# Optimization experiments

Measured on AMD Instinct MI355X. Metric: run time of the kernel, lower is better.

Reference implementation:

```python
import jax, jax.numpy as jnp
import numpy as np

B, N, DIN = 1, 1024, 512
NF, DCOND, H = 4, 128, 8
HD = DIN // H


def layernorm(x, g, b, eps=1e-5):
    mu = jnp.mean(x, axis=-1, keepdims=True)
    var = jnp.var(x, axis=-1, keepdims=True)
    return (x - mu) * jax.lax.rsqrt(var + eps) * g + b


def modlin2d(x, code, w_c, ln_g, ln_b, W, b):
    # code: [dcond, nf]; w_c: [din, dcond] -> code_mod: [nf, 1, din]
    code_mod = layernorm((w_c @ code).T, ln_g, ln_b)[:, None, :]
    return jnp.matmul(x * code_mod, W.T) + b


def setup_inputs() -> dict:
    key = jax.random.key(0)
    ks = jax.random.split(key, 8)
    s = lambda d: 1.0 / np.sqrt(d)
    return {
        "x": jax.random.normal(ks[0], (B, N, DIN), jnp.float32),
        "compatibility": jax.random.uniform(ks[1], (B, NF, N), jnp.float32),
        "code": jax.random.normal(ks[2], (DCOND, NF), jnp.float32),
        "w_c": jax.random.normal(ks[3], (DIN, DCOND), jnp.float32) * s(DCOND),
        "W_qkv": jax.random.normal(ks[4], (3 * DIN, DIN), jnp.float32) * s(DIN),
        "b_qkv": jnp.zeros((3 * DIN,), jnp.float32),
        "W_proj": jax.random.normal(ks[5], (DIN, DIN), jnp.float32) * s(DIN),
        "b_proj": jnp.zeros((DIN,), jnp.float32),
        "ln_qkv_g": jnp.ones((DIN,), jnp.float32),
        "ln_qkv_b": jnp.zeros((DIN,), jnp.float32),
        "ln_proj_g": jnp.ones((DIN,), jnp.float32),
        "ln_proj_b": jnp.zeros((DIN,), jnp.float32),
    }


def reference(x, compatibility, code, w_c, W_qkv, b_qkv, W_proj, b_proj,
              ln_qkv_g, ln_qkv_b, ln_proj_g, ln_proj_b):
    b, n, e = x.shape
    hd = e // H
    scale = hd ** -0.5
    # QKV: [B, nf, N, 3*din] -> split into [3, B, H, nf, N, hd]
    qkv = modlin2d(x[:, None, :, :], code, w_c, ln_qkv_g, ln_qkv_b, W_qkv, b_qkv)
    qkv = qkv.reshape(b, NF, n, 3, H, hd).transpose(3, 0, 4, 1, 2, 5)
    q, k, v = qkv[0], qkv[1], qkv[2]
    # first softmax over scaled scores
    attn = jax.nn.softmax(jnp.einsum('bhfnd,bhfmd->bhfnm', q, k) * scale, axis=-1)
    # compatibility outer product: [B, N, N] (sums over function axis)
    compat = jnp.einsum('bfn,bfm->bnm', compatibility, compatibility)
    W_hat = attn * compat[:, None, None, :, :]
    # second softmax
    Wm = jax.nn.softmax(W_hat, axis=-1)
    y_hat = jnp.einsum('bhfnm,bhfmd->bhfnd', Wm, v)
    y_hat = y_hat.transpose(0, 2, 3, 1, 4).reshape(b, NF, n, e)
    y = modlin2d(y_hat, code, w_c, ln_proj_g, ln_proj_b, W_proj, b_proj)
    return y
```

## Files before the change

kernel.cpp:

```cpp
#include <hip/hip_runtime.h>
#include <hip/hip_bf16.h>
#include <math.h>

#define NTOK 1024
#define DIN  512
#define NF   4
#define DCOND 128
#define H    8
#define HD   64
#define NQKV 1536

typedef __attribute__((ext_vector_type(8))) short bf16x8;
typedef __attribute__((ext_vector_type(4))) float f32x4;
typedef __attribute__((ext_vector_type(4))) unsigned short us4;

__device__ __forceinline__ unsigned short f2b(float f) {
  union { float f; unsigned int u; } v; v.f = f;
  unsigned int r = v.u + 0x7fffu + ((v.u >> 16) & 1u);
  return (unsigned short)(r >> 16);
}

__device__ __forceinline__ float b2f(unsigned short h) {
  union { unsigned int u; float f; } v; v.u = ((unsigned int)h) << 16;
  return v.f;
}

__device__ __forceinline__ void gl_lds16(const void* g, void* l) {
  __builtin_amdgcn_global_load_lds(
      (const __attribute__((address_space(1))) unsigned int*)g,
      (__attribute__((address_space(3))) unsigned int*)l, 16, 0, 0);
}

__global__ void ln_kernel(const float* __restrict__ code, const float* __restrict__ w_c,
                          const float* __restrict__ lnqg, const float* __restrict__ lnqb,
                          const float* __restrict__ lnpg, const float* __restrict__ lnpb,
                          float* __restrict__ cmq, float* __restrict__ cmp_) {
  const int i = threadIdx.x;
  const int w = i >> 6, lane = i & 63;
  float t[NF] = {0.f, 0.f, 0.f, 0.f};
  const float* wr = w_c + i * DCOND;
#pragma unroll 8
  for (int k = 0; k < DCOND; k += 4) {
    float4 wv = *reinterpret_cast<const float4*>(wr + k);
    float4 c0 = *reinterpret_cast<const float4*>(&code[k * 4]);
    float4 c1 = *reinterpret_cast<const float4*>(&code[(k + 1) * 4]);
    float4 c2 = *reinterpret_cast<const float4*>(&code[(k + 2) * 4]);
    float4 c3 = *reinterpret_cast<const float4*>(&code[(k + 3) * 4]);
    t[0] += wv.x * c0.x + wv.y * c1.x + wv.z * c2.x + wv.w * c3.x;
    t[1] += wv.x * c0.y + wv.y * c1.y + wv.z * c2.y + wv.w * c3.y;
    t[2] += wv.x * c0.z + wv.y * c1.z + wv.z * c2.z + wv.w * c3.z;
    t[3] += wv.x * c0.w + wv.y * c1.w + wv.z * c2.w + wv.w * c3.w;
  }
  __shared__ float redS[8], redQ[8];
#pragma unroll
  for (int f = 0; f < NF; ++f) {
    float s = t[f], q = t[f] * t[f];
#pragma unroll
    for (int o = 32; o > 0; o >>= 1) { s += __shfl_xor(s, o); q += __shfl_xor(q, o); }
    if (lane == 0) { redS[w] = s; redQ[w] = q; }
    __syncthreads();
    float S = 0.f, Q = 0.f;
#pragma unroll
    for (int j = 0; j < 8; ++j) { S += redS[j]; Q += redQ[j]; }
    float mu = S * (1.f / 512.f);
    float var = Q * (1.f / 512.f) - mu * mu;
    float rstd = rsqrtf(var + 1e-5f);
    float nv = (t[f] - mu) * rstd;
    cmq[f * DIN + i]  = nv * lnqg[i] + lnqb[i];
    cmp_[f * DIN + i] = nv * lnpg[i] + lnpb[i];
    __syncthreads();
  }
}

__global__ void prep2_kernel(const float* __restrict__ W_qkv, const float* __restrict__ W_proj,
                             const float* __restrict__ x, const float* __restrict__ cmq,
                             unsigned short* __restrict__ Wqh, unsigned short* __restrict__ Wph,
                             unsigned short* __restrict__ xm) {
  const int bid = blockIdx.x, tid = threadIdx.x;
  if (bid < 256) {
    const float* src; unsigned short* dst; int e;
    if (bid < 192) { src = W_qkv; dst = Wqh; e = bid * 4096 + tid * 16; }
    else { src = W_proj; dst = Wph; e = (bid - 192) * 4096 + tid * 16; }
#pragma unroll
    for (int j = 0; j < 4; ++j) {
      float4 a = *reinterpret_cast<const float4*>(&src[e + j * 4]);
      us4 p = { f2b(a.x), f2b(a.y), f2b(a.z), f2b(a.w) };
      *reinterpret_cast<us4*>(&dst[e + j * 4]) = p;
    }
  } else {
    int e = (bid - 256) * 4096 + tid * 16;
    int row = e >> 9, d = e & 511;
    int f = row >> 10, n = row & 1023;
    const float* xr = x + (size_t)n * DIN + d;
    const float* cr = cmq + f * DIN + d;
#pragma unroll
    for (int j = 0; j < 4; ++j) {
      float4 a = *reinterpret_cast<const float4*>(xr + j * 4);
      float4 c = *reinterpret_cast<const float4*>(cr + j * 4);
      us4 p = { f2b(a.x * c.x), f2b(a.y * c.y), f2b(a.z * c.z), f2b(a.w * c.w) };
      *reinterpret_cast<us4*>(&xm[e + j * 4]) = p;
    }
  }
}

template<int NCOL, bool OUT_BF16, bool WRITE_VT>
__global__ __launch_bounds__(256, 3)
void gemm_bb(const unsigned short* __restrict__ Ah,
             const unsigned short* __restrict__ Wh,
             const float* __restrict__ bias,
             unsigned short* __restrict__ outH,
             float* __restrict__ outF,
             unsigned short* __restrict__ vT) {
  __shared__ __align__(16) unsigned short sA[2][4096];
  __shared__ __align__(16) unsigned short sB[2][4096];
  const int tid = threadIdx.x;
  const int lane = tid & 63, w = tid >> 6;
  const int li = lane & 15, g = lane >> 4;
  const int wr = (w >> 1) * 64, wc = (w & 1) * 64;
  const int row0 = blockIdx.y * 128, col0 = blockIdx.x * 128;
  const int f = row0 >> 10;

  f32x4 acc[4][4];
#pragma unroll
  for (int m = 0; m < 4; ++m)
#pragma unroll
    for (int n = 0; n < 4; ++n) acc[m][n] = (f32x4){0.f, 0.f, 0.f, 0.f};

  auto stage = [&](int buf, int k0) {
#pragma unroll
    for (int j = 0; j < 2; ++j) {
      int slot = w * 128 + j * 64 + lane;
      int r = slot >> 2, sp = slot & 3, s = sp ^ ((r >> 1) & 3);
      gl_lds16(Ah + (size_t)(row0 + r) * DIN + k0 + s * 8, &sA[buf][(w * 128 + j * 64) * 8]);
    }
#pragma unroll
    for (int j = 0; j < 2; ++j) {
      int slot = w * 128 + j * 64 + lane;
      int r = slot >> 2, sp = slot & 3, s = sp ^ ((r >> 1) & 3);
      gl_lds16(Wh + (size_t)(col0 + r) * DIN + k0 + s * 8, &sB[buf][(w * 128 + j * 64) * 8]);
    }
  };

  stage(0, 0);
  __syncthreads();
  for (int it = 0; it < 16; ++it) {
    int buf = it & 1;
    if (it < 15) stage(buf ^ 1, (it + 1) * 32);
    bf16x8 aF[4], bF[4];
#pragma unroll
    for (int m = 0; m < 4; ++m) {
      int ra = wr + m * 16 + li;
      aF[m] = *reinterpret_cast<const bf16x8*>(&sA[buf][(ra * 4 + (g ^ ((ra >> 1) & 3))) * 8]);
    }
#pragma unroll
    for (int n = 0; n < 4; ++n) {
      int cb = wc + n * 16 + li;
      bF[n] = *reinterpret_cast<const bf16x8*>(&sB[buf][(cb * 4 + (g ^ ((cb >> 1) & 3))) * 8]);
    }
#pragma unroll
    for (int m = 0; m < 4; ++m)
#pragma unroll
      for (int n = 0; n < 4; ++n)
        acc[m][n] = __builtin_amdgcn_mfma_f32_16x16x32_bf16(aF[m], bF[n], acc[m][n], 0, 0, 0);
    __syncthreads();
  }
#pragma unroll
  for (int n = 0; n < 4; ++n) {
    int col = col0 + wc + n * 16 + li;
    float bb = bias[col];
#pragma unroll
    for (int m = 0; m < 4; ++m) {
      int rb = row0 + wr + m * 16 + g * 4;
      f32x4 v = acc[m][n];
      if constexpr (OUT_BF16) {
        if (WRITE_VT && col >= 1024) {
          int tok0 = rb & 1023;
          us4 pk;
#pragma unroll
          for (int r = 0; r < 4; ++r) pk[r] = f2b(v[r] + bb);
          *reinterpret_cast<us4*>(&vT[((size_t)(f * 512 + (col - 1024))) * NTOK + tok0]) = pk;
        } else {
#pragma unroll
          for (int r = 0; r < 4; ++r)
            outH[(size_t)(rb + r) * NCOL + col] = f2b(v[r] + bb);
        }
      } else {
#pragma unroll
        for (int r = 0; r < 4; ++r)
          outF[(size_t)(rb + r) * NCOL + col] = v[r] + bb;
      }
    }
  }
}

__global__ __launch_bounds__(256, 3)
void attn_mfma(const unsigned short* __restrict__ qkvh,
               const unsigned short* __restrict__ vTh,
               const float* __restrict__ comp,
               const float* __restrict__ cmp_,
               unsigned short* __restrict__ ym) {
  __shared__ __align__(16) unsigned short sK[2][4096];
  __shared__ __align__(16) unsigned short sVT[2][4096];
  __shared__ __align__(16) unsigned short sW[4][16 * 72];
  __shared__ __align__(16) unsigned short scompH[4096];
  const int tid = threadIdx.x, lane = tid & 63, w = tid >> 6;
  const int li = lane & 15, g = lane >> 4;
  const int hf = blockIdx.x;
  const int qt = blockIdx.y;
  const int h = hf >> 2, f = hf & 3;

  {
    int e = tid * 16;
#pragma unroll
    for (int j = 0; j < 4; ++j) {
      float4 a = *reinterpret_cast<const float4*>(&comp[e + j * 4]);
      us4 p = { f2b(a.x), f2b(a.y), f2b(a.z), f2b(a.w) };
      *reinterpret_cast<us4*>(&scompH[e + j * 4]) = p;
    }
  }

  const int qrow0 = qt * 64 + w * 16;
  const unsigned short* qbase = qkvh + ((size_t)(f * NTOK + qrow0 + li)) * NQKV + h * HD;
  bf16x8 aq[2];
  aq[0] = *reinterpret_cast<const bf16x8*>(qbase + g * 8);
  aq[1] = *reinterpret_cast<const bf16x8*>(qbase + 32 + g * 8);

  float crow[4][4];
#pragma unroll
  for (int ff = 0; ff < 4; ++ff)
#pragma unroll
    for (int r = 0; r < 4; ++r)
      crow[ff][r] = comp[ff * NTOK + qrow0 + g * 4 + r];

  const unsigned short* kb = qkvh + ((size_t)(f * NTOK)) * NQKV + DIN + h * HD;
  const unsigned short* vb = vTh + ((size_t)(f * DIN + h * HD)) * NTOK;

  auto stage_k = [&](int buf, int t) {
#pragma unroll
    for (int j = 0; j < 2; ++j) {
      int slot = w * 128 + j * 64 + lane;
      int tok = slot >> 3, sp = slot & 7, s = sp ^ (tok & 7);
      gl_lds16(kb + (size_t)(t * 64 + tok) * NQKV + s * 8, &sK[buf][(w * 128 + j * 64) * 8]);
    }
  };
  auto stage_v = [&](int buf, int t) {
#pragma unroll
    for (int j = 0; j < 2; ++j) {
      int slot = w * 128 + j * 64 + lane;
      int d = slot >> 3, sp = slot & 7, s = sp ^ (d & 7);
      gl_lds16(vb + (size_t)d * NTOK + t * 64 + s * 8, &sVT[buf][(w * 128 + j * 64) * 8]);
    }
  };

  float mrow[4], lrow[4];
#pragma unroll
  for (int r = 0; r < 4; ++r) { mrow[r] = -1e30f; lrow[r] = 0.f; }

  stage_k(0, 0);
  __syncthreads();
  for (int t = 0; t < 16; ++t) {
    int buf = t & 1;
    if (t < 15) stage_k(buf ^ 1, t + 1);
    bf16x8 bk[4][2];
#pragma unroll
    for (int cf = 0; cf < 4; ++cf)
#pragma unroll
      for (int ks = 0; ks < 2; ++ks) {
        int tok = cf * 16 + li, s = ks * 4 + g;
        bk[cf][ks] = *reinterpret_cast<const bf16x8*>(&sK[buf][(tok * 8 + (s ^ (tok & 7))) * 8]);
      }
    f32x4 accs[4];
#pragma unroll
    for (int cf = 0; cf < 4; ++cf) accs[cf] = (f32x4){0.f, 0.f, 0.f, 0.f};
#pragma unroll
    for (int ks = 0; ks < 2; ++ks)
#pragma unroll
      for (int cf = 0; cf < 4; ++cf)
        accs[cf] = __builtin_amdgcn_mfma_f32_16x16x32_bf16(aq[ks], bk[cf][ks], accs[cf], 0, 0, 0);
#pragma unroll
    for (int r = 0; r < 4; ++r) {
      float v0 = accs[0][r] * 0.125f, v1 = accs[1][r] * 0.125f;
      float v2 = accs[2][r] * 0.125f, v3 = accs[3][r] * 0.125f;
      float tm = fmaxf(fmaxf(v0, v1), fmaxf(v2, v3));
#pragma unroll
      for (int o = 8; o > 0; o >>= 1) tm = fmaxf(tm, __shfl_xor(tm, o));
      float nm = fmaxf(mrow[r], tm);
      float ssum = __expf(v0 - nm) + __expf(v1 - nm) + __expf(v2 - nm) + __expf(v3 - nm);
#pragma unroll
      for (int o = 8; o > 0; o >>= 1) ssum += __shfl_xor(ssum, o);
      lrow[r] = lrow[r] * __expf(mrow[r] - nm) + ssum;
      mrow[r] = nm;
    }
    __syncthreads();
  }
  float inv_l[4];
#pragma unroll
  for (int r = 0; r < 4; ++r) inv_l[r] = 1.f / lrow[r];

  f32x4 acco[4];
  float sum2[4] = {0.f, 0.f, 0.f, 0.f};
#pragma unroll
  for (int cf = 0; cf < 4; ++cf) acco[cf] = (f32x4){0.f, 0.f, 0.f, 0.f};
  unsigned short* wbuf = &sW[w][0];

  stage_k(0, 0);
  stage_v(0, 0);
  __syncthreads();
  for (int t = 0; t < 16; ++t) {
    int buf = t & 1;
    if (t < 15) { stage_k(buf ^ 1, t + 1); stage_v(buf ^ 1, t + 1); }
    bf16x8 bk[4][2];
#pragma unroll
    for (int cf = 0; cf < 4; ++cf)
#pragma unroll
      for (int ks = 0; ks < 2; ++ks) {
        int tok = cf * 16 + li, s = ks * 4 + g;
        bk[cf][ks] = *reinterpret_cast<const bf16x8*>(&sK[buf][(tok * 8 + (s ^ (tok & 7))) * 8]);
      }
    f32x4 accs[4];
#pragma unroll
    for (int cf = 0; cf < 4; ++cf) accs[cf] = (f32x4){0.f, 0.f, 0.f, 0.f};
#pragma unroll
    for (int ks = 0; ks < 2; ++ks)
#pragma unroll
      for (int cf = 0; cf < 4; ++cf)
        accs[cf] = __builtin_amdgcn_mfma_f32_16x16x32_bf16(aq[ks], bk[cf][ks], accs[cf], 0, 0, 0);
#pragma unroll
    for (int cf = 0; cf < 4; ++cf) {
      int col = t * 64 + cf * 16 + li;
      float c0 = b2f(scompH[col]), c1 = b2f(scompH[1024 + col]);
      float c2 = b2f(scompH[2048 + col]), c3 = b2f(scompH[3072 + col]);
#pragma unroll
      for (int r = 0; r < 4; ++r) {
        float v = accs[cf][r] * 0.125f;
        float a = __expf(v - mrow[r]) * inv_l[r];
        float cc = crow[0][r] * c0 + crow[1][r] * c1 + crow[2][r] * c2 + crow[3][r] * c3;
        float tv = __expf(a * cc);
        unsigned short hv = f2b(tv);
        sum2[r] += b2f(hv);
        wbuf[(g * 4 + r) * 72 + cf * 16 + li] = hv;
      }
    }
    bf16x8 aw[2], bv[4][2];
#pragma unroll
    for (int ks = 0; ks < 2; ++ks)
      aw[ks] = *reinterpret_cast<const bf16x8*>(&wbuf[li * 72 + ks * 32 + g * 8]);
#pragma unroll
    for (int cf = 0; cf < 4; ++cf)
#pragma unroll
      for (int ks = 0; ks < 2; ++ks) {
        int d = cf * 16 + li, s = ks * 4 + g;
        bv[cf][ks] = *reinterpret_cast<const bf16x8*>(&sVT[buf][(d * 8 + (s ^ (d & 7))) * 8]);
      }
#pragma unroll
    for (int ks = 0; ks < 2; ++ks)
#pragma unroll
      for (int cf = 0; cf < 4; ++cf)
        acco[cf] = __builtin_amdgcn_mfma_f32_16x16x32_bf16(aw[ks], bv[cf][ks], acco[cf], 0, 0, 0);
    __syncthreads();
  }
#pragma unroll
  for (int r = 0; r < 4; ++r) {
#pragma unroll
    for (int o = 8; o > 0; o >>= 1) sum2[r] += __shfl_xor(sum2[r], o);
  }
  float cscale[4];
#pragma unroll
  for (int cf = 0; cf < 4; ++cf) cscale[cf] = cmp_[f * DIN + h * HD + cf * 16 + li];
#pragma unroll
  for (int cf = 0; cf < 4; ++cf)
#pragma unroll
    for (int r = 0; r < 4; ++r) {
      int qrow = qrow0 + g * 4 + r;
      ym[((size_t)(f * NTOK + qrow)) * DIN + h * HD + cf * 16 + li] =
          f2b(acco[cf][r] / sum2[r] * cscale[cf]);
    }
}

extern "C" void kernel_launch(void* const* d_in, const int* in_sizes, int n_in,
                              void* d_out, int out_size, void* d_ws, size_t ws_size,
                              hipStream_t stream) {
  const float* x      = (const float*)d_in[0];
  const float* compat = (const float*)d_in[1];
  const float* code   = (const float*)d_in[2];
  const float* w_c    = (const float*)d_in[3];
  const float* W_qkv  = (const float*)d_in[4];
  const float* b_qkv  = (const float*)d_in[5];
  const float* W_proj = (const float*)d_in[6];
  const float* b_proj = (const float*)d_in[7];
  const float* lnqg   = (const float*)d_in[8];
  const float* lnqb   = (const float*)d_in[9];
  const float* lnpg   = (const float*)d_in[10];
  const float* lnpb   = (const float*)d_in[11];
  float* out = (float*)d_out;

  float* cmq  = (float*)d_ws;
  float* cmp_ = cmq + NF * DIN;
  unsigned short* Wqh  = (unsigned short*)(cmp_ + NF * DIN);
  unsigned short* Wph  = Wqh + (size_t)NQKV * DIN;
  unsigned short* xm   = Wph + (size_t)DIN * DIN;
  unsigned short* qkvh = xm + (size_t)NF * NTOK * DIN;
  unsigned short* vTh  = qkvh + (size_t)NF * NTOK * NQKV;
  unsigned short* ym   = vTh + (size_t)NF * DIN * NTOK;

  ln_kernel<<<1, 512, 0, stream>>>(code, w_c, lnqg, lnqb, lnpg, lnpb, cmq, cmp_);
  prep2_kernel<<<768, 256, 0, stream>>>(W_qkv, W_proj, x, cmq, Wqh, Wph, xm);
  gemm_bb<NQKV, true, true><<<dim3(12, 32), 256, 0, stream>>>(
      xm, Wqh, b_qkv, qkvh, nullptr, vTh);
  attn_mfma<<<dim3(32, 16), 256, 0, stream>>>(qkvh, vTh, compat, cmp_, ym);
  gemm_bb<DIN, false, false><<<dim3(4, 32), 256, 0, stream>>>(
      ym, Wph, b_proj, nullptr, out, nullptr);
}
```

Baseline: 174.0 us.

## Split attention key range across wave pairs, shrink GEMM tiles, drop max tracking

The attention kernel now gives each block 32 query rows and splits the key range between two wave groups. Partial row sums and outputs are reduced through shared memory, and the grid doubles to fill more CUs. The online max tracking in the first softmax pass is removed and the 1/8 scale is folded into Q in the QKV GEMM epilogue, which relies on scores staying small enough not to overflow exp. The GEMMs use 64x64 tiles for more blocks and occupancy, and compatibility values are packed two bf16 per word in LDS.

```diff
diff --git a/kernel.cpp b/kernel.cpp
--- a/kernel.cpp
+++ b/kernel.cpp
@@ -22,6 +22,11 @@
 
 __device__ __forceinline__ float b2f(unsigned short h) {
   union { unsigned int u; float f; } v; v.u = ((unsigned int)h) << 16;
+  return v.f;
+}
+
+__device__ __forceinline__ float asf(unsigned int u) {
+  union { unsigned int u; float f; } v; v.u = u;
   return v.f;
 }
 
@@ -103,73 +108,68 @@
   }
 }
 
-template<int NCOL, bool OUT_BF16, bool WRITE_VT>
-__global__ __launch_bounds__(256, 3)
-void gemm_bb(const unsigned short* __restrict__ Ah,
-             const unsigned short* __restrict__ Wh,
-             const float* __restrict__ bias,
-             unsigned short* __restrict__ outH,
-             float* __restrict__ outF,
-             unsigned short* __restrict__ vT) {
-  __shared__ __align__(16) unsigned short sA[2][4096];
-  __shared__ __align__(16) unsigned short sB[2][4096];
+template<int NCOL, bool OUT_BF16, bool WRITE_VT, bool SCALE_Q>
+__global__ __launch_bounds__(256, 6)
+void gemm64(const unsigned short* __restrict__ Ah,
+            const unsigned short* __restrict__ Wh,
+            const float* __restrict__ bias,
+            unsigned short* __restrict__ outH,
+            float* __restrict__ outF,
+            unsigned short* __restrict__ vT) {
+  __shared__ __align__(16) unsigned short sA[2][2048];
+  __shared__ __align__(16) unsigned short sB[2][2048];
   const int tid = threadIdx.x;
   const int lane = tid & 63, w = tid >> 6;
   const int li = lane & 15, g = lane >> 4;
-  const int wr = (w >> 1) * 64, wc = (w & 1) * 64;
-  const int row0 = blockIdx.y * 128, col0 = blockIdx.x * 128;
+  const int wr = (w >> 1) * 32, wc = (w & 1) * 32;
+  const int row0 = blockIdx.y * 64, col0 = blockIdx.x * 64;
   const int f = row0 >> 10;
-
-  f32x4 acc[4][4];
-#pragma unroll
-  for (int m = 0; m < 4; ++m)
-#pragma unroll
-    for (int n = 0; n < 4; ++n) acc[m][n] = (f32x4){0.f, 0.f, 0.f, 0.f};
-
-  auto stage = [&](int buf, int k0) {
-#pragma unroll
-    for (int j = 0; j < 2; ++j) {
-      int slot = w * 128 + j * 64 + lane;
-      int r = slot >> 2, sp = slot & 3, s = sp ^ ((r >> 1) & 3);
-      gl_lds16(Ah + (size_t)(row0 + r) * DIN + k0 + s * 8, &sA[buf][(w * 128 + j * 64) * 8]);
-    }
-#pragma unroll
-    for (int j = 0; j < 2; ++j) {
-      int slot = w * 128 + j * 64 + lane;
-      int r = slot >> 2, sp = slot & 3, s = sp ^ ((r >> 1) & 3);
-      gl_lds16(Wh + (size_t)(col0 + r) * DIN + k0 + s * 8, &sB[buf][(w * 128 + j * 64) * 8]);
-    }
-  };
-
-  stage(0, 0);
+  const int sr = tid >> 2, sp = tid & 3;
+  const int ss = sp ^ ((sr >> 1) & 3);
+
+  f32x4 acc[2][2];
+#pragma unroll
+  for (int m = 0; m < 2; ++m)
+#pragma unroll
+    for (int n = 0; n < 2; ++n) acc[m][n] = (f32x4){0.f, 0.f, 0.f, 0.f};
+
+  const unsigned short* aSrc = Ah + (size_t)(row0 + sr) * DIN + ss * 8;
+  const unsigned short* bSrc = Wh + (size_t)(col0 + sr) * DIN + ss * 8;
+
+  gl_lds16(aSrc, &sA[0][w * 512]);
+  gl_lds16(bSrc, &sB[0][w * 512]);
   __syncthreads();
   for (int it = 0; it < 16; ++it) {
     int buf = it & 1;
-    if (it < 15) stage(buf ^ 1, (it + 1) * 32);
-    bf16x8 aF[4], bF[4];
-#pragma unroll
-    for (int m = 0; m < 4; ++m) {
+    if (it < 15) {
+      gl_lds16(aSrc + (it + 1) * 32, &sA[buf ^ 1][w * 512]);
+      gl_lds16(bSrc + (it + 1) * 32, &sB[buf ^ 1][w * 512]);
+    }
+    bf16x8 aF[2], bF[2];
+#pragma unroll
+    for (int m = 0; m < 2; ++m) {
       int ra = wr + m * 16 + li;
       aF[m] = *reinterpret_cast<const bf16x8*>(&sA[buf][(ra * 4 + (g ^ ((ra >> 1) & 3))) * 8]);
     }
 #pragma unroll
-    for (int n = 0; n < 4; ++n) {
+    for (int n = 0; n < 2; ++n) {
       int cb = wc + n * 16 + li;
       bF[n] = *reinterpret_cast<const bf16x8*>(&sB[buf][(cb * 4 + (g ^ ((cb >> 1) & 3))) * 8]);
     }
 #pragma unroll
-    for (int m = 0; m < 4; ++m)
-#pragma unroll
-      for (int n = 0; n < 4; ++n)
+    for (int m = 0; m < 2; ++m)
+#pragma unroll
+      for (int n = 0; n < 2; ++n)
         acc[m][n] = __builtin_amdgcn_mfma_f32_16x16x32_bf16(aF[m], bF[n], acc[m][n], 0, 0, 0);
     __syncthreads();
   }
 #pragma unroll
-  for (int n = 0; n < 4; ++n) {
+  for (int n = 0; n < 2; ++n) {
     int col = col0 + wc + n * 16 + li;
     float bb = bias[col];
-#pragma unroll
-    for (int m = 0; m < 4; ++m) {
+    float sc = (SCALE_Q && col < DIN) ? 0.125f : 1.0f;
+#pragma unroll
+    for (int m = 0; m < 2; ++m) {
       int rb = row0 + wr + m * 16 + g * 4;
       f32x4 v = acc[m][n];
       if constexpr (OUT_BF16) {
@@ -182,7 +182,7 @@
         } else {
 #pragma unroll
           for (int r = 0; r < 4; ++r)
-            outH[(size_t)(rb + r) * NCOL + col] = f2b(v[r] + bb);
+            outH[(size_t)(rb + r) * NCOL + col] = f2b((v[r] + bb) * sc);
         }
       } else {
 #pragma unroll
@@ -194,32 +194,40 @@
 }
 
 __global__ __launch_bounds__(256, 3)
-void attn_mfma(const unsigned short* __restrict__ qkvh,
-               const unsigned short* __restrict__ vTh,
-               const float* __restrict__ comp,
-               const float* __restrict__ cmp_,
-               unsigned short* __restrict__ ym) {
+void attn_mfma2(const unsigned short* __restrict__ qkvh,
+                const unsigned short* __restrict__ vTh,
+                const float* __restrict__ comp,
+                const float* __restrict__ cmp_,
+                unsigned short* __restrict__ ym) {
   __shared__ __align__(16) unsigned short sK[2][4096];
-  __shared__ __align__(16) unsigned short sVT[2][4096];
+  __shared__ __align__(16) unsigned short sV[2][4096];
   __shared__ __align__(16) unsigned short sW[4][16 * 72];
-  __shared__ __align__(16) unsigned short scompH[4096];
+  __shared__ unsigned int sc01[1024], sc23[1024];
+  __shared__ float lred[2][2][16];
+  __shared__ float s2red[2][16];
   const int tid = threadIdx.x, lane = tid & 63, w = tid >> 6;
   const int li = lane & 15, g = lane >> 4;
-  const int hf = blockIdx.x;
-  const int qt = blockIdx.y;
+  const int rt = w & 1, ch = w >> 1;
+  const int hf = blockIdx.x, qt = blockIdx.y;
   const int h = hf >> 2, f = hf & 3;
 
   {
-    int e = tid * 16;
-#pragma unroll
-    for (int j = 0; j < 4; ++j) {
-      float4 a = *reinterpret_cast<const float4*>(&comp[e + j * 4]);
-      us4 p = { f2b(a.x), f2b(a.y), f2b(a.z), f2b(a.w) };
-      *reinterpret_cast<us4*>(&scompH[e + j * 4]) = p;
-    }
-  }
-
-  const int qrow0 = qt * 64 + w * 16;
+    int c = tid * 4;
+    float4 a0 = *reinterpret_cast<const float4*>(&comp[c]);
+    float4 a1 = *reinterpret_cast<const float4*>(&comp[1024 + c]);
+    float4 a2 = *reinterpret_cast<const float4*>(&comp[2048 + c]);
+    float4 a3 = *reinterpret_cast<const float4*>(&comp[3072 + c]);
+    sc01[c + 0] = f2b(a0.x) | ((unsigned int)f2b(a1.x) << 16);
+    sc01[c + 1] = f2b(a0.y) | ((unsigned int)f2b(a1.y) << 16);
+    sc01[c + 2] = f2b(a0.z) | ((unsigned int)f2b(a1.z) << 16);
+    sc01[c + 3] = f2b(a0.w) | ((unsigned int)f2b(a1.w) << 16);
+    sc23[c + 0] = f2b(a2.x) | ((unsigned int)f2b(a3.x) << 16);
+    sc23[c + 1] = f2b(a2.y) | ((unsigned int)f2b(a3.y) << 16);
+    sc23[c + 2] = f2b(a2.z) | ((unsigned int)f2b(a3.z) << 16);
+    sc23[c + 3] = f2b(a2.w) | ((unsigned int)f2b(a3.w) << 16);
+  }
+
+  const int qrow0 = qt * 32 + rt * 16;
   const unsigned short* qbase = qkvh + ((size_t)(f * NTOK + qrow0 + li)) * NQKV + h * HD;
   bf16x8 aq[2];
   aq[0] = *reinterpret_cast<const bf16x8*>(qbase + g * 8);
@@ -235,39 +243,39 @@
   const unsigned short* kb = qkvh + ((size_t)(f * NTOK)) * NQKV + DIN + h * HD;
   const unsigned short* vb = vTh + ((size_t)(f * DIN + h * HD)) * NTOK;
 
-  auto stage_k = [&](int buf, int t) {
-#pragma unroll
-    for (int j = 0; j < 2; ++j) {
-      int slot = w * 128 + j * 64 + lane;
+  auto stageK = [&](unsigned short* dst, int t) {
+#pragma unroll
+    for (int j = 0; j < 8; ++j) {
+      int slot = j * 64 + lane;
       int tok = slot >> 3, sp = slot & 7, s = sp ^ (tok & 7);
-      gl_lds16(kb + (size_t)(t * 64 + tok) * NQKV + s * 8, &sK[buf][(w * 128 + j * 64) * 8]);
+      gl_lds16(kb + (size_t)(t * 64 + tok) * NQKV + s * 8, dst + j * 512);
     }
   };
-  auto stage_v = [&](int buf, int t) {
-#pragma unroll
-    for (int j = 0; j < 2; ++j) {
-      int slot = w * 128 + j * 64 + lane;
+  auto stageV = [&](unsigned short* dst, int t) {
+#pragma unroll
+    for (int j = 0; j < 8; ++j) {
+      int slot = j * 64 + lane;
       int d = slot >> 3, sp = slot & 7, s = sp ^ (d & 7);
-      gl_lds16(vb + (size_t)d * NTOK + t * 64 + s * 8, &sVT[buf][(w * 128 + j * 64) * 8]);
+      gl_lds16(vb + (size_t)d * NTOK + t * 64 + s * 8, dst + j * 512);
     }
   };
 
-  float mrow[4], lrow[4];
-#pragma unroll
-  for (int r = 0; r < 4; ++r) { mrow[r] = -1e30f; lrow[r] = 0.f; }
-
-  stage_k(0, 0);
+  float lsum[4] = {0.f, 0.f, 0.f, 0.f};
+  stageK(sK[ch], ch * 8);
   __syncthreads();
-  for (int t = 0; t < 16; ++t) {
-    int buf = t & 1;
-    if (t < 15) stage_k(buf ^ 1, t + 1);
+  for (int tt = 0; tt < 8; ++tt) {
+    unsigned short* cur = (tt & 1) ? sV[ch] : sK[ch];
+    if (tt < 7) {
+      unsigned short* nxt = (tt & 1) ? sK[ch] : sV[ch];
+      stageK(nxt, ch * 8 + tt + 1);
+    }
     bf16x8 bk[4][2];
 #pragma unroll
     for (int cf = 0; cf < 4; ++cf)
 #pragma unroll
       for (int ks = 0; ks < 2; ++ks) {
         int tok = cf * 16 + li, s = ks * 4 + g;
-        bk[cf][ks] = *reinterpret_cast<const bf16x8*>(&sK[buf][(tok * 8 + (s ^ (tok & 7))) * 8]);
+        bk[cf][ks] = *reinterpret_cast<const bf16x8*>(&cur[(tok * 8 + (s ^ (tok & 7))) * 8]);
       }
     f32x4 accs[4];
 #pragma unroll
@@ -278,24 +286,27 @@
       for (int cf = 0; cf < 4; ++cf)
         accs[cf] = __builtin_amdgcn_mfma_f32_16x16x32_bf16(aq[ks], bk[cf][ks], accs[cf], 0, 0, 0);
 #pragma unroll
-    for (int r = 0; r < 4; ++r) {
-      float v0 = accs[0][r] * 0.125f, v1 = accs[1][r] * 0.125f;
-      float v2 = accs[2][r] * 0.125f, v3 = accs[3][r] * 0.125f;
-      float tm = fmaxf(fmaxf(v0, v1), fmaxf(v2, v3));
-#pragma unroll
-      for (int o = 8; o > 0; o >>= 1) tm = fmaxf(tm, __shfl_xor(tm, o));
-      float nm = fmaxf(mrow[r], tm);
-      float ssum = __expf(v0 - nm) + __expf(v1 - nm) + __expf(v2 - nm) + __expf(v3 - nm);
-#pragma unroll
-      for (int o = 8; o > 0; o >>= 1) ssum += __shfl_xor(ssum, o);
-      lrow[r] = lrow[r] * __expf(mrow[r] - nm) + ssum;
-      mrow[r] = nm;
-    }
-    __syncthreads();
-  }
-  float inv_l[4];
-#pragma unroll
-  for (int r = 0; r < 4; ++r) inv_l[r] = 1.f / lrow[r];
+    for (int cf = 0; cf < 4; ++cf)
+#pragma unroll
+      for (int r = 0; r < 4; ++r) lsum[r] += __expf(accs[cf][r]);
+    __syncthreads();
+  }
+#pragma unroll
+  for (int r = 0; r < 4; ++r) {
+    lsum[r] += __shfl_xor(lsum[r], 1);
+    lsum[r] += __shfl_xor(lsum[r], 2);
+    lsum[r] += __shfl_xor(lsum[r], 4);
+    lsum[r] += __shfl_xor(lsum[r], 8);
+  }
+  if (li == 0) {
+#pragma unroll
+    for (int r = 0; r < 4; ++r) lred[ch][rt][g * 4 + r] = lsum[r];
+  }
+  __syncthreads();
+  float invl[4];
+#pragma unroll
+  for (int r = 0; r < 4; ++r)
+    invl[r] = 1.f / (lred[0][rt][g * 4 + r] + lred[1][rt][g * 4 + r]);
 
   f32x4 acco[4];
   float sum2[4] = {0.f, 0.f, 0.f, 0.f};
@@ -303,19 +314,18 @@
   for (int cf = 0; cf < 4; ++cf) acco[cf] = (f32x4){0.f, 0.f, 0.f, 0.f};
   unsigned short* wbuf = &sW[w][0];
 
-  stage_k(0, 0);
-  stage_v(0, 0);
-  __syncthreads();
-  for (int t = 0; t < 16; ++t) {
-    int buf = t & 1;
-    if (t < 15) { stage_k(buf ^ 1, t + 1); stage_v(buf ^ 1, t + 1); }
+  for (int tt = 0; tt < 8; ++tt) {
+    int t = ch * 8 + tt;
+    stageK(sK[ch], t);
+    stageV(sV[ch], t);
+    __syncthreads();
     bf16x8 bk[4][2];
 #pragma unroll
     for (int cf = 0; cf < 4; ++cf)
 #pragma unroll
       for (int ks = 0; ks < 2; ++ks) {
         int tok = cf * 16 + li, s = ks * 4 + g;
-        bk[cf][ks] = *reinterpret_cast<const bf16x8*>(&sK[buf][(tok * 8 + (s ^ (tok & 7))) * 8]);
+        bk[cf][ks] = *reinterpret_cast<const bf16x8*>(&sK[ch][(tok * 8 + (s ^ (tok & 7))) * 8]);
       }
     f32x4 accs[4];
 #pragma unroll
@@ -327,13 +337,13 @@
         accs[cf] = __builtin_amdgcn_mfma_f32_16x16x32_bf16(aq[ks], bk[cf][ks], accs[cf], 0, 0, 0);
 #pragma unroll
     for (int cf = 0; cf < 4; ++cf) {
-      int col = t * 64 + cf * 16 + li;
-      float c0 = b2f(scompH[col]), c1 = b2f(scompH[1024 + col]);
-      float c2 = b2f(scompH[2048 + col]), c3 = b2f(scompH[3072 + col]);
+      int colg = t * 64 + cf * 16 + li;
+      unsigned int u01 = sc01[colg], u23 = sc23[colg];
+      float c0 = asf(u01 << 16), c1 = asf(u01 & 0xffff0000u);
+      float c2 = asf(u23 << 16), c3 = asf(u23 & 0xffff0000u);
 #pragma unroll
       for (int r = 0; r < 4; ++r) {
-        float v = accs[cf][r] * 0.125f;
-        float a = __expf(v - mrow[r]) * inv_l[r];
+        float a = __expf(accs[cf][r]) * invl[r];
         float cc = crow[0][r] * c0 + crow[1][r] * c1 + crow[2][r] * c2 + crow[3][r] * c3;
         float tv = __expf(a * cc);
         unsigned short hv = f2b(tv);
@@ -341,7 +351,7 @@
         wbuf[(g * 4 + r) * 72 + cf * 16 + li] = hv;
       }
     }
-    bf16x8 aw[2], bv[4][2];
+    bf16x8 aw[2], bv2[4][2];
 #pragma unroll
     for (int ks = 0; ks < 2; ++ks)
       aw[ks] = *reinterpret_cast<const bf16x8*>(&wbuf[li * 72 + ks * 32 + g * 8]);
@@ -350,31 +360,52 @@
 #pragma unroll
       for (int ks = 0; ks < 2; ++ks) {
         int d = cf * 16 + li, s = ks * 4 + g;
-        bv[cf][ks] = *reinterpret_cast<const bf16x8*>(&sVT[buf][(d * 8 + (s ^ (d & 7))) * 8]);
+        bv2[cf][ks] = *reinterpret_cast<const bf16x8*>(&sV[ch][(d * 8 + (s ^ (d & 7))) * 8]);
       }
 #pragma unroll
     for (int ks = 0; ks < 2; ++ks)
 #pragma unroll
       for (int cf = 0; cf < 4; ++cf)
-        acco[cf] = __builtin_amdgcn_mfma_f32_16x16x32_bf16(aw[ks], bv[cf][ks], acco[cf], 0, 0, 0);
-    __syncthreads();
-  }
+        acco[cf] = __builtin_amdgcn_mfma_f32_16x16x32_bf16(aw[ks], bv2[cf][ks], acco[cf], 0, 0, 0);
+    __syncthreads();
+  }
+
 #pragma unroll
   for (int r = 0; r < 4; ++r) {
-#pragma unroll
-    for (int o = 8; o > 0; o >>= 1) sum2[r] += __shfl_xor(sum2[r], o);
-  }
-  float cscale[4];
-#pragma unroll
-  for (int cf = 0; cf < 4; ++cf) cscale[cf] = cmp_[f * DIN + h * HD + cf * 16 + li];
-#pragma unroll
-  for (int cf = 0; cf < 4; ++cf)
-#pragma unroll
-    for (int r = 0; r < 4; ++r) {
-      int qrow = qrow0 + g * 4 + r;
-      ym[((size_t)(f * NTOK + qrow)) * DIN + h * HD + cf * 16 + li] =
-          f2b(acco[cf][r] / sum2[r] * cscale[cf]);
-    }
+    sum2[r] += __shfl_xor(sum2[r], 1);
+    sum2[r] += __shfl_xor(sum2[r], 2);
+    sum2[r] += __shfl_xor(sum2[r], 4);
+    sum2[r] += __shfl_xor(sum2[r], 8);
+  }
+  float* fred = (float*)sK;
+  if (ch == 1) {
+    if (li == 0) {
+#pragma unroll
+      for (int r = 0; r < 4; ++r) s2red[rt][g * 4 + r] = sum2[r];
+    }
+#pragma unroll
+    for (int cf = 0; cf < 4; ++cf)
+#pragma unroll
+      for (int r = 0; r < 4; ++r)
+        fred[rt * 1024 + (g * 4 + r) * 64 + cf * 16 + li] = acco[cf][r];
+  }
+  __syncthreads();
+  if (ch == 0) {
+    float invs[4];
+#pragma unroll
+    for (int r = 0; r < 4; ++r) invs[r] = 1.f / (sum2[r] + s2red[rt][g * 4 + r]);
+    float cscale[4];
+#pragma unroll
+    for (int cf = 0; cf < 4; ++cf) cscale[cf] = cmp_[f * DIN + h * HD + cf * 16 + li];
+#pragma unroll
+    for (int cf = 0; cf < 4; ++cf)
+#pragma unroll
+      for (int r = 0; r < 4; ++r) {
+        float v = (acco[cf][r] + fred[rt * 1024 + (g * 4 + r) * 64 + cf * 16 + li]) * invs[r];
+        int qrow = qrow0 + g * 4 + r;
+        ym[((size_t)(f * NTOK + qrow)) * DIN + h * HD + cf * 16 + li] = f2b(v * cscale[cf]);
+      }
+  }
 }
 
 extern "C" void kernel_launch(void* const* d_in, const int* in_sizes, int n_in,
@@ -405,9 +436,9 @@
 
   ln_kernel<<<1, 512, 0, stream>>>(code, w_c, lnqg, lnqb, lnpg, lnpb, cmq, cmp_);
   prep2_kernel<<<768, 256, 0, stream>>>(W_qkv, W_proj, x, cmq, Wqh, Wph, xm);
-  gemm_bb<NQKV, true, true><<<dim3(12, 32), 256, 0, stream>>>(
+  gemm64<NQKV, true, true, true><<<dim3(24, 64), 256, 0, stream>>>(
       xm, Wqh, b_qkv, qkvh, nullptr, vTh);
-  attn_mfma<<<dim3(32, 16), 256, 0, stream>>>(qkvh, vTh, compat, cmp_, ym);
-  gemm_bb<DIN, false, false><<<dim3(4, 32), 256, 0, stream>>>(
+  attn_mfma2<<<dim3(32, 32), 256, 0, stream>>>(qkvh, vTh, compat, cmp_, ym);
+  gemm64<DIN, false, false, false><<<dim3(8, 64), 256, 0, stream>>>(
       ym, Wph, b_proj, nullptr, out, nullptr);
 }
```

After: 173.7 us. No clear change (-0.2%).
